# Kernel tuning notes

Hardware: AMD Instinct MI355X
Metric: run time of the kernel (lower is better)

Reference implementation:

```python
import jax, jax.numpy as jnp
import numpy as np
import math

B, H, W, D = 4, 64, 64, 256
N, K, V = 8, 32, 32


def setup_inputs() -> dict:
    key = jax.random.key(0)
    ks = jax.random.split(key, 7)
    blob = jax.random.normal(ks[0], (B, H, W, D), dtype=jnp.float32)
    # 1x1 conv kernels == dense [D, out] matrices; glorot-ish scale
    s = 1.0 / math.sqrt(D)
    wq = jax.random.normal(ks[1], (D, N * K), dtype=jnp.float32) * s
    wk = jax.random.normal(ks[2], (D, N * K), dtype=jnp.float32) * s
    wv = jax.random.normal(ks[3], (D, N * V), dtype=jnp.float32) * s
    bq = jnp.zeros((N * K,), jnp.float32)
    bk = jnp.zeros((N * K,), jnp.float32)
    bv = jnp.zeros((N * V,), jnp.float32)
    return {"blob": blob, "wq": wq, "bq": bq, "wk": wk, "bk": bk, "wv": wv, "bv": bv}


def _maxpool2x2(x):
    # MaxPool2D with pool_size=strides=(2,2), VALID padding, NHWC
    return jax.lax.reduce_window(
        x, -jnp.inf, jax.lax.max,
        window_dimensions=(1, 2, 2, 1), window_strides=(1, 2, 2, 1), padding="VALID")


def reference(blob, wq, bq, wk, bk, wv, bv):
    H2, W2 = H // 2, W // 2
    # pooled query path
    q = _maxpool2x2(blob)                                   # [B,H2,W2,D]
    q = (q @ wq + bq).reshape(B, H2, W2, N, K)              # [B,H2,W2,N,K]
    q = q * (1.0 / math.sqrt(float(K)))
    # key/value paths (1x1 conv == per-pixel matmul); swish on value
    k = (blob @ wk + bk).reshape(B, H * W, N, K)            # [B,HW,N,K]
    v = jax.nn.swish(blob @ wv + bv).reshape(B, H * W, N, V)  # [B,HW,N,V]
    # cross-attention: contract K, outer product of pooled grid with full grid
    scores = jnp.einsum("bhwnk,bink->bhwin", q, k)          # [B,H2,W2,HW,N]
    attn = jax.nn.softmax(scores, axis=3)                   # softmax over HW
    out = jnp.einsum("bhwin,binv->bhwnv", attn, v)          # [B,H2,W2,N,V]
    return out.reshape(B, H2, W2, N * V)
```

## Files before the change

### kernel.cpp

```cpp
#include <hip/hip_runtime.h>


typedef _Float16 f16x8 __attribute__((ext_vector_type(8)));
typedef _Float16 f16x4 __attribute__((ext_vector_type(4)));
typedef float    f32x4 __attribute__((ext_vector_type(4)));

#define F16(x) static_cast<_Float16>(x)

#if __has_builtin(__builtin_amdgcn_exp2f)
#define EXP2(x) __builtin_amdgcn_exp2f(x)
#else
#define EXP2(x) exp2f(x)
#endif

__device__ __forceinline__ void gl_lds16(const void* g, void* l) {
    __builtin_amdgcn_global_load_lds(
        (const __attribute__((address_space(1))) unsigned int*)g,
        (__attribute__((address_space(3))) unsigned int*)l, 16, 0, 0);
}

__global__ __launch_bounds__(256) void prep_kernel(
    const float* __restrict__ wq, const float* __restrict__ wk,
    const float* __restrict__ wv, _Float16* __restrict__ wt) {
    __shared__ float t[32][33];
    const int blk = blockIdx.x;
    const int mat = blk >> 6;
    const int tile = blk & 63;
    const int d0 = (tile >> 3) * 32, o0 = (tile & 7) * 32;
    const float* w = (mat == 0) ? wq : (mat == 1 ? wk : wv);
    const int tx = threadIdx.x & 31, ty = threadIdx.x >> 5;
#pragma unroll
    for (int i = 0; i < 4; ++i)
        t[ty + i * 8][tx] = w[(d0 + ty + i * 8) * 256 + o0 + tx];
    __syncthreads();
#pragma unroll
    for (int i = 0; i < 4; ++i)
        wt[(mat << 16) + (o0 + ty + i * 8) * 256 + d0 + tx] = (_Float16)t[tx][ty + i * 8];
}

__global__ __launch_bounds__(256) void proj_kernel(
    const float* __restrict__ blob, const _Float16* __restrict__ wt,
    const float* __restrict__ bq, const float* __restrict__ bk, const float* __restrict__ bv,
    _Float16* __restrict__ qo, _Float16* __restrict__ ko, _Float16* __restrict__ vo) {
    __shared__ __align__(16) char atile[2][4096];

    const int tid = threadIdx.x;
    const int lane = tid & 63, wid = tid >> 6;
    const int quad = lane >> 4, l16 = lane & 15;
    int jb = blockIdx.x;
    int job, rowblk;
    if (jb < 64)       { job = 0; rowblk = jb; }
    else if (jb < 320) { job = 1; rowblk = jb - 64; }
    else               { job = 2; rowblk = jb - 320; }
    const int rowbase = rowblk * 64;
    const int colbase = wid * 64;
    const _Float16* wmat = wt + ((size_t)job << 16);
    const float* bias = (job == 0) ? bq : (job == 1 ? bk : bv);

    const int srow = tid >> 2, sc8 = tid & 3;
    const int sslot = srow * 4 + ((sc8 + (srow >> 2)) & 3);
    const float* aptr;
    if (job == 0) {
        const int grow = rowbase + srow;
        const int bb = grow >> 10, y = (grow >> 5) & 31, x = grow & 31;
        aptr = blob + (((bb * 64 + 2 * y) * 64) + 2 * x) * 256 + sc8 * 8;
    } else {
        aptr = blob + (size_t)(rowbase + srow) * 256 + sc8 * 8;
    }

    const _Float16* wptr[4];
#pragma unroll
    for (int nt = 0; nt < 4; ++nt)
        wptr[nt] = wmat + (size_t)(colbase + nt * 16 + l16) * 256 + quad * 8;

    const int aread = l16 * 64 + ((quad + (l16 >> 2)) & 3) * 16;

    f32x4 acc[4][4];
#pragma unroll
    for (int mc = 0; mc < 4; ++mc)
#pragma unroll
        for (int nt = 0; nt < 4; ++nt) acc[mc][nt] = (f32x4){0.f, 0.f, 0.f, 0.f};

    f16x8 wf[2][4];
    float4 ar[2][2];

    auto A_LOAD = [&](int t, float4* dst) {
        const float* p = aptr + t * 32;
        if (job == 0) {
            float4 a0 = *(const float4*)(p);
            float4 a1 = *(const float4*)(p + 4);
            float4 b0 = *(const float4*)(p + 256);
            float4 b1 = *(const float4*)(p + 260);
            float4 c0 = *(const float4*)(p + 16384);
            float4 c1 = *(const float4*)(p + 16388);
            float4 d0 = *(const float4*)(p + 16640);
            float4 d1 = *(const float4*)(p + 16644);
            dst[0].x = fmaxf(fmaxf(a0.x, b0.x), fmaxf(c0.x, d0.x));
            dst[0].y = fmaxf(fmaxf(a0.y, b0.y), fmaxf(c0.y, d0.y));
            dst[0].z = fmaxf(fmaxf(a0.z, b0.z), fmaxf(c0.z, d0.z));
            dst[0].w = fmaxf(fmaxf(a0.w, b0.w), fmaxf(c0.w, d0.w));
            dst[1].x = fmaxf(fmaxf(a1.x, b1.x), fmaxf(c1.x, d1.x));
            dst[1].y = fmaxf(fmaxf(a1.y, b1.y), fmaxf(c1.y, d1.y));
            dst[1].z = fmaxf(fmaxf(a1.z, b1.z), fmaxf(c1.z, d1.z));
            dst[1].w = fmaxf(fmaxf(a1.w, b1.w), fmaxf(c1.w, d1.w));
        } else {
            dst[0] = *(const float4*)(p);
            dst[1] = *(const float4*)(p + 4);
        }
    };
    auto A_WRITE = [&](int buf, const float4* src) {
        auto c0 = __builtin_amdgcn_cvt_pkrtz(src[0].x, src[0].y);
        auto c1 = __builtin_amdgcn_cvt_pkrtz(src[0].z, src[0].w);
        auto c2 = __builtin_amdgcn_cvt_pkrtz(src[1].x, src[1].y);
        auto c3 = __builtin_amdgcn_cvt_pkrtz(src[1].z, src[1].w);
        f16x8 v = {F16(c0[0]), F16(c0[1]), F16(c1[0]), F16(c1[1]),
                   F16(c2[0]), F16(c2[1]), F16(c3[0]), F16(c3[1])};
        *(f16x8*)(atile[buf] + sslot * 16) = v;
    };
    auto W_LOAD = [&](int t, f16x8* dst) {
#pragma unroll
        for (int nt = 0; nt < 4; ++nt) dst[nt] = *(const f16x8*)(wptr[nt] + t * 32);
    };

    W_LOAD(0, wf[0]);
    A_LOAD(0, ar[0]);
    A_WRITE(0, ar[0]);
    A_LOAD(1, ar[1]);
    asm volatile("s_waitcnt lgkmcnt(0)\n\ts_barrier" ::: "memory");

#pragma unroll
    for (int s = 0; s < 8; ++s) {
        if (s < 7) W_LOAD(s + 1, wf[(s + 1) & 1]);
        f16x8 af[4];
#pragma unroll
        for (int mc = 0; mc < 4; ++mc)
            af[mc] = *(const f16x8*)(atile[s & 1] + mc * 1024 + aread);
#pragma unroll
        for (int mc = 0; mc < 4; ++mc)
#pragma unroll
            for (int nt = 0; nt < 4; ++nt)
                acc[mc][nt] = __builtin_amdgcn_mfma_f32_16x16x32_f16(
                    af[mc], wf[s & 1][nt], acc[mc][nt], 0, 0, 0);
        if (s < 7) A_WRITE((s + 1) & 1, ar[(s + 1) & 1]);
        if (s < 6) A_LOAD(s + 2, ar[s & 1]);
        if (s < 7) asm volatile("s_waitcnt lgkmcnt(0)\n\ts_barrier" ::: "memory");
    }

#pragma unroll
    for (int nt = 0; nt < 4; ++nt) {
        const int o = colbase + nt * 16 + l16;
        const float bs = bias[o];
        const int nh = o >> 5, kk = o & 31;
#pragma unroll
        for (int mc = 0; mc < 4; ++mc) {
            if (job == 0) {
#pragma unroll
                for (int r = 0; r < 4; ++r) {
                    const int grow = rowbase + mc * 16 + quad * 4 + r;
                    const float x = (acc[mc][nt][r] + bs) * 0.25503508f;
                    const int bb = grow >> 10, mm = grow & 1023;
                    qo[(((bb * 8 + nh) * 1024 + mm) << 5) + kk] = (_Float16)x;
                }
            } else if (job == 1) {
#pragma unroll
                for (int r = 0; r < 4; ++r) {
                    const int grow = rowbase + mc * 16 + quad * 4 + r;
                    const float x = acc[mc][nt][r] + bs;
                    const int bb = grow >> 12, ii = grow & 4095;
                    ko[(((bb * 8 + nh) * 4096 + ii) << 5) + kk] = (_Float16)x;
                }
            } else {
                const int grow0 = rowbase + mc * 16 + quad * 4;
                const int bb = grow0 >> 12, i0 = grow0 & 4095;
                f16x4 pv;
#pragma unroll
                for (int r = 0; r < 4; ++r) {
                    float x = acc[mc][nt][r] + bs;
                    const float sg = 1.0f / (1.0f + __expf(-x));
                    pv[r] = (_Float16)(x * sg);
                }
                *(f16x4*)(vo + (((size_t)(bb * 8 + nh) * 32 + kk) << 12) + i0) = pv;
            }
        }
    }
}

__global__ __launch_bounds__(512, 4) void attn_kernel(
    const _Float16* __restrict__ qb,
    const _Float16* __restrict__ kb,
    const _Float16* __restrict__ vt,
    float* __restrict__ out) {
    __shared__ __align__(16) char pool[49152];

    const int tid = threadIdx.x;
    const int lane = tid & 63, wid = tid >> 6;
    const int quad = lane >> 4, l16 = lane & 15;
    const int bn = blockIdx.x & 31, mt = blockIdx.x >> 5;
    const int b = bn >> 3, n = bn & 7;
    const int m0 = mt * 64;
    const int rg = wid & 3, kc = wid >> 2;

    const _Float16* gsrc[2];
    int ldsoff[2], adv[2];
#pragma unroll
    for (int jj = 0; jj < 2; ++jj) {
        const int j = wid + jj * 8;
        const int kcj = j >> 3, sub = j & 7;
        const int gl = (sub & 3) * 64 + lane;
        if (sub < 4) {
            const int k = gl >> 2, c = ((gl & 3) - (k >> 2)) & 3;
            gsrc[jj]   = kb + ((size_t)bn << 17) + (size_t)(kcj * 2048 + k) * 32 + c * 8;
            ldsoff[jj] = kcj * 24576 + gl * 16;
            adv[jj] = 2048;
        } else {
            const int v = gl >> 3, c = ((gl & 7) - v) & 7;
            gsrc[jj]   = vt + ((size_t)bn << 17) + (size_t)v * 4096 + kcj * 2048 + c * 8;
            ldsoff[jj] = kcj * 24576 + 4096 + gl * 16;
            adv[jj] = 64;
        }
    }

    const f16x8 qf = *(const f16x8*)(qb + (((size_t)(bn << 10) + m0 + rg * 16 + l16) << 5) + quad * 8);

    const int kread = kc * 24576 + l16 * 64 + ((quad + (l16 >> 2)) & 3) * 16;
    const int vread = kc * 24576 + 4096 + l16 * 128 + (quad & 1) * 8;
    const int r0 = (quad >> 1) + l16;

#pragma unroll
    for (int p = 0; p < 2; ++p)
#pragma unroll
        for (int jj = 0; jj < 2; ++jj) {
            gl_lds16(gsrc[jj], pool + ldsoff[jj] + p * 8192);
            gsrc[jj] += adv[jj];
        }
    asm volatile("s_waitcnt vmcnt(2)\n\ts_barrier" ::: "memory");

    f32x4 acc0 = (f32x4){0.f, 0.f, 0.f, 0.f};
    f32x4 acc1 = acc0;
    float ps0 = 0.f;

    for (int s = 0; s < 32; ++s) {
        if (s < 30) {
            const int nb = ((s + 2) % 3) * 8192;
#pragma unroll
            for (int jj = 0; jj < 2; ++jj) {
                gl_lds16(gsrc[jj], pool + ldsoff[jj] + nb);
                gsrc[jj] += adv[jj];
            }
        }
        const char* kbase = pool + kread + (s % 3) * 8192;
        const char* vbase = pool + vread + (s % 3) * 8192;
#pragma unroll
        for (int tloc = 0; tloc < 4; ++tloc) {
            const f16x8 kf = *(const f16x8*)(kbase + tloc * 1024);
            const int rot = ((2 * tloc + r0) & 7) * 16;
            const f16x4 va0 = *(const f16x4*)(vbase + rot);
            const f16x4 va1 = *(const f16x4*)(vbase + rot + 2048);

            f32x4 s0 = __builtin_amdgcn_mfma_f32_16x16x32_f16(kf, qf, (f32x4){0.f,0.f,0.f,0.f}, 0, 0, 0);
            const float p0 = EXP2(s0[0]), p1 = EXP2(s0[1]), p2 = EXP2(s0[2]), p3 = EXP2(s0[3]);
            ps0 += (p0 + p1) + (p2 + p3);
            auto e0 = __builtin_amdgcn_cvt_pkrtz(p0, p1);
            auto e1 = __builtin_amdgcn_cvt_pkrtz(p2, p3);
            const f16x4 pb = {F16(e0[0]), F16(e0[1]), F16(e1[0]), F16(e1[1])};
            acc0 = __builtin_amdgcn_mfma_f32_16x16x16f16(va0, pb, acc0, 0, 0, 0);
            acc1 = __builtin_amdgcn_mfma_f32_16x16x16f16(va1, pb, acc1, 0, 0, 0);
        }
        if (s < 30)       asm volatile("s_waitcnt vmcnt(2)\n\ts_barrier" ::: "memory");
        else if (s == 30) asm volatile("s_waitcnt vmcnt(0)\n\ts_barrier" ::: "memory");
        else              asm volatile("s_barrier" ::: "memory");
    }

    float* num = (float*)pool;
    float* den = (float*)(pool + 64 * 33 * 4);
    for (int i = tid; i < 64 * 33 + 64; i += 512) ((float*)pool)[i] = 0.f;
    __syncthreads();

    ps0 += __shfl_xor(ps0, 16); ps0 += __shfl_xor(ps0, 32);

    const int m = rg * 16 + l16;
#pragma unroll
    for (int r = 0; r < 4; ++r) {
        atomicAdd(&num[m * 33 + quad * 4 + r], acc0[r]);
        atomicAdd(&num[m * 33 + 16 + quad * 4 + r], acc1[r]);
    }
    if (quad == 0) atomicAdd(&den[m], ps0);
    __syncthreads();

    {
        const int mloc = tid >> 3, v4 = (tid & 7) * 4;
        const float inv = 1.0f / den[mloc];
        const float* nr = num + mloc * 33 + v4;
        float4 o = {nr[0] * inv, nr[1] * inv, nr[2] * inv, nr[3] * inv};
        *(float4*)(out + (((size_t)(b << 10) + m0 + mloc) << 8) + n * 32 + v4) = o;
    }
}

extern "C" void kernel_launch(void* const* d_in, const int* in_sizes, int n_in,
                              void* d_out, int out_size, void* d_ws, size_t ws_size,
                              hipStream_t stream) {
    const float* blob = (const float*)d_in[0];
    const float* wq = (const float*)d_in[1];
    const float* bq = (const float*)d_in[2];
    const float* wk = (const float*)d_in[3];
    const float* bk = (const float*)d_in[4];
    const float* wv = (const float*)d_in[5];
    const float* bv = (const float*)d_in[6];
    float* out = (float*)d_out;

    char* ws = (char*)d_ws;
    _Float16* wt = (_Float16*)(ws);
    _Float16* ko = (_Float16*)(ws + 393216);
    _Float16* vo = (_Float16*)(ws + 8781824);
    _Float16* qo = (_Float16*)(ws + 17170432);

    prep_kernel<<<192, 256, 0, stream>>>(wq, wk, wv, wt);
    proj_kernel<<<576, 256, 0, stream>>>(blob, wt, bq, bk, bv, qo, ko, vo);
    attn_kernel<<<512, 512, 0, stream>>>(qo, ko, vo, out);
}
```

Measured before the change: 137.2 us.

## Give each wave a private key slice and pre-swizzle V into fragment layout

The projection kernel now writes V directly in the per-lane MFMA fragment order. Each attention wave then owns a contiguous 512-key slice and streams it through its own 4-stage LDS ring. Each wave processes all four 16-row query groups against its K/V tile, so the per-step block-wide barriers are replaced by per-wave vmcnt waits, and fragments are read with single 16-byte loads. This adds accumulator registers and 64KB of LDS per block, which may lower occupancy.

```diff
diff --git a/kernel.cpp b/kernel.cpp
--- a/kernel.cpp
+++ b/kernel.cpp
@@ -179,7 +179,8 @@
                     const float sg = 1.0f / (1.0f + __expf(-x));
                     pv[r] = (_Float16)(x * sg);
                 }
-                *(f16x4*)(vo + (((size_t)(bb * 8 + nh) * 32 + kk) << 12) + i0) = pv;
+                *(f16x4*)(vo + (size_t)(bb * 8 + nh) * 131072 + (i0 >> 4) * 512
+                             + ((kk & 15) + quad * 16) * 8 + (kk >> 4) * 4) = pv;
             }
         }
     }
@@ -188,9 +189,9 @@
 __global__ __launch_bounds__(512, 4) void attn_kernel(
     const _Float16* __restrict__ qb,
     const _Float16* __restrict__ kb,
-    const _Float16* __restrict__ vt,
+    const _Float16* __restrict__ vf,
     float* __restrict__ out) {
-    __shared__ __align__(16) char pool[49152];
+    __shared__ __align__(16) char pool[65536];
 
     const int tid = threadIdx.x;
     const int lane = tid & 63, wid = tid >> 6;
@@ -198,93 +199,88 @@
     const int bn = blockIdx.x & 31, mt = blockIdx.x >> 5;
     const int b = bn >> 3, n = bn & 7;
     const int m0 = mt * 64;
-    const int rg = wid & 3, kc = wid >> 2;
-
-    const _Float16* gsrc[2];
-    int ldsoff[2], adv[2];
-#pragma unroll
-    for (int jj = 0; jj < 2; ++jj) {
-        const int j = wid + jj * 8;
-        const int kcj = j >> 3, sub = j & 7;
-        const int gl = (sub & 3) * 64 + lane;
-        if (sub < 4) {
-            const int k = gl >> 2, c = ((gl & 3) - (k >> 2)) & 3;
-            gsrc[jj]   = kb + ((size_t)bn << 17) + (size_t)(kcj * 2048 + k) * 32 + c * 8;
-            ldsoff[jj] = kcj * 24576 + gl * 16;
-            adv[jj] = 2048;
+    const int key0 = wid << 9;
+
+    char* const lds0 = pool + wid * 8192;
+
+    const _Float16* kp = kb + ((size_t)bn << 17)
+                            + (size_t)(key0 + (lane & 15)) * 32 + (lane >> 4) * 8;
+    const _Float16* vp = vf + ((size_t)bn << 17) + (size_t)(key0 >> 4) * 512 + lane * 8;
+
+    f16x8 qf[4];
+#pragma unroll
+    for (int rg = 0; rg < 4; ++rg)
+        qf[rg] = *(const f16x8*)(qb + (((size_t)(bn << 10) + m0 + rg * 16 + l16) << 5) + quad * 8);
+
+#pragma unroll
+    for (int p = 0; p < 3; ++p) {
+        gl_lds16(kp, lds0 + p * 2048);        kp += 512;
+        gl_lds16(vp, lds0 + p * 2048 + 1024); vp += 512;
+    }
+
+    f32x4 acc[4][2];
+#pragma unroll
+    for (int rg = 0; rg < 4; ++rg) {
+        acc[rg][0] = (f32x4){0.f, 0.f, 0.f, 0.f};
+        acc[rg][1] = acc[rg][0];
+    }
+    float ps[4] = {0.f, 0.f, 0.f, 0.f};
+
+#pragma unroll 4
+    for (int s = 0; s < 32; ++s) {
+        if (s < 29) {
+            char* nb = lds0 + ((s + 3) & 3) * 2048;
+            gl_lds16(kp, nb);        kp += 512;
+            gl_lds16(vp, nb + 1024); vp += 512;
+            asm volatile("s_waitcnt vmcnt(6)" ::: "memory");
+        } else if (s == 29) {
+            asm volatile("s_waitcnt vmcnt(4)" ::: "memory");
+        } else if (s == 30) {
+            asm volatile("s_waitcnt vmcnt(2)" ::: "memory");
         } else {
-            const int v = gl >> 3, c = ((gl & 7) - v) & 7;
-            gsrc[jj]   = vt + ((size_t)bn << 17) + (size_t)v * 4096 + kcj * 2048 + c * 8;
-            ldsoff[jj] = kcj * 24576 + 4096 + gl * 16;
-            adv[jj] = 64;
-        }
-    }
-
-    const f16x8 qf = *(const f16x8*)(qb + (((size_t)(bn << 10) + m0 + rg * 16 + l16) << 5) + quad * 8);
-
-    const int kread = kc * 24576 + l16 * 64 + ((quad + (l16 >> 2)) & 3) * 16;
-    const int vread = kc * 24576 + 4096 + l16 * 128 + (quad & 1) * 8;
-    const int r0 = (quad >> 1) + l16;
-
-#pragma unroll
-    for (int p = 0; p < 2; ++p)
-#pragma unroll
-        for (int jj = 0; jj < 2; ++jj) {
-            gl_lds16(gsrc[jj], pool + ldsoff[jj] + p * 8192);
-            gsrc[jj] += adv[jj];
-        }
-    asm volatile("s_waitcnt vmcnt(2)\n\ts_barrier" ::: "memory");
-
-    f32x4 acc0 = (f32x4){0.f, 0.f, 0.f, 0.f};
-    f32x4 acc1 = acc0;
-    float ps0 = 0.f;
-
-    for (int s = 0; s < 32; ++s) {
-        if (s < 30) {
-            const int nb = ((s + 2) % 3) * 8192;
-#pragma unroll
-            for (int jj = 0; jj < 2; ++jj) {
-                gl_lds16(gsrc[jj], pool + ldsoff[jj] + nb);
-                gsrc[jj] += adv[jj];
-            }
-        }
-        const char* kbase = pool + kread + (s % 3) * 8192;
-        const char* vbase = pool + vread + (s % 3) * 8192;
-#pragma unroll
-        for (int tloc = 0; tloc < 4; ++tloc) {
-            const f16x8 kf = *(const f16x8*)(kbase + tloc * 1024);
-            const int rot = ((2 * tloc + r0) & 7) * 16;
-            const f16x4 va0 = *(const f16x4*)(vbase + rot);
-            const f16x4 va1 = *(const f16x4*)(vbase + rot + 2048);
-
-            f32x4 s0 = __builtin_amdgcn_mfma_f32_16x16x32_f16(kf, qf, (f32x4){0.f,0.f,0.f,0.f}, 0, 0, 0);
+            asm volatile("s_waitcnt vmcnt(0)" ::: "memory");
+        }
+        const char* base = lds0 + (s & 3) * 2048;
+        const f16x8 kf = *(const f16x8*)(base + lane * 16);
+        const f16x8 vv = *(const f16x8*)(base + 1024 + lane * 16);
+        const f16x4 va0 = {vv[0], vv[1], vv[2], vv[3]};
+        const f16x4 va1 = {vv[4], vv[5], vv[6], vv[7]};
+#pragma unroll
+        for (int rg = 0; rg < 4; ++rg) {
+            f32x4 s0 = __builtin_amdgcn_mfma_f32_16x16x32_f16(kf, qf[rg], (f32x4){0.f,0.f,0.f,0.f}, 0, 0, 0);
             const float p0 = EXP2(s0[0]), p1 = EXP2(s0[1]), p2 = EXP2(s0[2]), p3 = EXP2(s0[3]);
-            ps0 += (p0 + p1) + (p2 + p3);
+            ps[rg] += (p0 + p1) + (p2 + p3);
             auto e0 = __builtin_amdgcn_cvt_pkrtz(p0, p1);
             auto e1 = __builtin_amdgcn_cvt_pkrtz(p2, p3);
             const f16x4 pb = {F16(e0[0]), F16(e0[1]), F16(e1[0]), F16(e1[1])};
-            acc0 = __builtin_amdgcn_mfma_f32_16x16x16f16(va0, pb, acc0, 0, 0, 0);
-            acc1 = __builtin_amdgcn_mfma_f32_16x16x16f16(va1, pb, acc1, 0, 0, 0);
-        }
-        if (s < 30)       asm volatile("s_waitcnt vmcnt(2)\n\ts_barrier" ::: "memory");
-        else if (s == 30) asm volatile("s_waitcnt vmcnt(0)\n\ts_barrier" ::: "memory");
-        else              asm volatile("s_barrier" ::: "memory");
-    }
-
+            acc[rg][0] = __builtin_amdgcn_mfma_f32_16x16x16f16(va0, pb, acc[rg][0], 0, 0, 0);
+            acc[rg][1] = __builtin_amdgcn_mfma_f32_16x16x16f16(va1, pb, acc[rg][1], 0, 0, 0);
+        }
+    }
+
+    asm volatile("s_waitcnt vmcnt(0)" ::: "memory");
+    __syncthreads();
     float* num = (float*)pool;
     float* den = (float*)(pool + 64 * 33 * 4);
     for (int i = tid; i < 64 * 33 + 64; i += 512) ((float*)pool)[i] = 0.f;
     __syncthreads();
 
-    ps0 += __shfl_xor(ps0, 16); ps0 += __shfl_xor(ps0, 32);
-
-    const int m = rg * 16 + l16;
-#pragma unroll
-    for (int r = 0; r < 4; ++r) {
-        atomicAdd(&num[m * 33 + quad * 4 + r], acc0[r]);
-        atomicAdd(&num[m * 33 + 16 + quad * 4 + r], acc1[r]);
-    }
-    if (quad == 0) atomicAdd(&den[m], ps0);
+#pragma unroll
+    for (int rg = 0; rg < 4; ++rg) {
+        ps[rg] += __shfl_xor(ps[rg], 16);
+        ps[rg] += __shfl_xor(ps[rg], 32);
+    }
+
+#pragma unroll
+    for (int rg = 0; rg < 4; ++rg) {
+        const int m = rg * 16 + l16;
+#pragma unroll
+        for (int r = 0; r < 4; ++r) {
+            atomicAdd(&num[m * 33 + quad * 4 + r], acc[rg][0][r]);
+            atomicAdd(&num[m * 33 + 16 + quad * 4 + r], acc[rg][1][r]);
+        }
+        if (quad == 0) atomicAdd(&den[m], ps[rg]);
+    }
     __syncthreads();
 
     {
```

After: 162.3 us. +18.3%, slower.

## Store K and V in MFMA-fragment order so LDS reads are contiguous

Applied to the files above, without the earlier changes.

The projection kernel now writes V in a pre-swizzled fragment layout that matches the per-lane MFMA operand order. The attention kernel's async global-to-LDS copies become plain contiguous 1 KB chunks for K and V with a uniform advance, and each lane reads K and V with one 16-byte LDS load at lane*16 instead of rotated, swizzled addresses and two 8-byte V loads. This cuts address arithmetic and LDS read instructions in the inner loop. The trade-off is that the producer's scattered stores change pattern, and bank-conflict behaviour now depends on the linear lane layout.

```diff
diff --git a/kernel.cpp b/kernel.cpp
--- a/kernel.cpp
+++ b/kernel.cpp
@@ -179,7 +179,8 @@
                     const float sg = 1.0f / (1.0f + __expf(-x));
                     pv[r] = (_Float16)(x * sg);
                 }
-                *(f16x4*)(vo + (((size_t)(bb * 8 + nh) * 32 + kk) << 12) + i0) = pv;
+                *(f16x4*)(vo + (size_t)(bb * 8 + nh) * 131072 + (i0 >> 4) * 512
+                             + ((kk & 15) + quad * 16) * 8 + (kk >> 4) * 4) = pv;
             }
         }
     }
@@ -188,7 +189,7 @@
 __global__ __launch_bounds__(512, 4) void attn_kernel(
     const _Float16* __restrict__ qb,
     const _Float16* __restrict__ kb,
-    const _Float16* __restrict__ vt,
+    const _Float16* __restrict__ vf,
     float* __restrict__ out) {
     __shared__ __align__(16) char pool[49152];
 
@@ -201,37 +202,32 @@
     const int rg = wid & 3, kc = wid >> 2;
 
     const _Float16* gsrc[2];
-    int ldsoff[2], adv[2];
+    int ldsoff[2];
 #pragma unroll
     for (int jj = 0; jj < 2; ++jj) {
         const int j = wid + jj * 8;
         const int kcj = j >> 3, sub = j & 7;
-        const int gl = (sub & 3) * 64 + lane;
         if (sub < 4) {
-            const int k = gl >> 2, c = ((gl & 3) - (k >> 2)) & 3;
-            gsrc[jj]   = kb + ((size_t)bn << 17) + (size_t)(kcj * 2048 + k) * 32 + c * 8;
-            ldsoff[jj] = kcj * 24576 + gl * 16;
-            adv[jj] = 2048;
+            gsrc[jj] = kb + ((size_t)bn << 17)
+                     + (size_t)(kcj * 2048 + sub * 16 + (lane & 15)) * 32 + (lane >> 4) * 8;
+            ldsoff[jj] = kcj * 24576 + sub * 1024;
         } else {
-            const int v = gl >> 3, c = ((gl & 7) - v) & 7;
-            gsrc[jj]   = vt + ((size_t)bn << 17) + (size_t)v * 4096 + kcj * 2048 + c * 8;
-            ldsoff[jj] = kcj * 24576 + 4096 + gl * 16;
-            adv[jj] = 64;
+            gsrc[jj] = vf + ((size_t)bn << 17)
+                     + (size_t)(kcj * 128 + (sub - 4)) * 512 + lane * 8;
+            ldsoff[jj] = kcj * 24576 + 4096 + (sub - 4) * 1024;
         }
     }
 
     const f16x8 qf = *(const f16x8*)(qb + (((size_t)(bn << 10) + m0 + rg * 16 + l16) << 5) + quad * 8);
 
-    const int kread = kc * 24576 + l16 * 64 + ((quad + (l16 >> 2)) & 3) * 16;
-    const int vread = kc * 24576 + 4096 + l16 * 128 + (quad & 1) * 8;
-    const int r0 = (quad >> 1) + l16;
+    const int rbase = kc * 24576 + lane * 16;
 
 #pragma unroll
     for (int p = 0; p < 2; ++p)
 #pragma unroll
         for (int jj = 0; jj < 2; ++jj) {
             gl_lds16(gsrc[jj], pool + ldsoff[jj] + p * 8192);
-            gsrc[jj] += adv[jj];
+            gsrc[jj] += 2048;
         }
     asm volatile("s_waitcnt vmcnt(2)\n\ts_barrier" ::: "memory");
 
@@ -245,17 +241,16 @@
 #pragma unroll
             for (int jj = 0; jj < 2; ++jj) {
                 gl_lds16(gsrc[jj], pool + ldsoff[jj] + nb);
-                gsrc[jj] += adv[jj];
+                gsrc[jj] += 2048;
             }
         }
-        const char* kbase = pool + kread + (s % 3) * 8192;
-        const char* vbase = pool + vread + (s % 3) * 8192;
+        const char* base = pool + rbase + (s % 3) * 8192;
 #pragma unroll
         for (int tloc = 0; tloc < 4; ++tloc) {
-            const f16x8 kf = *(const f16x8*)(kbase + tloc * 1024);
-            const int rot = ((2 * tloc + r0) & 7) * 16;
-            const f16x4 va0 = *(const f16x4*)(vbase + rot);
-            const f16x4 va1 = *(const f16x4*)(vbase + rot + 2048);
+            const f16x8 kf = *(const f16x8*)(base + tloc * 1024);
+            const f16x8 vv = *(const f16x8*)(base + 4096 + tloc * 1024);
+            const f16x4 va0 = {vv[0], vv[1], vv[2], vv[3]};
+            const f16x4 va1 = {vv[4], vv[5], vv[6], vv[7]};
 
             f32x4 s0 = __builtin_amdgcn_mfma_f32_16x16x32_f16(kf, qf, (f32x4){0.f,0.f,0.f,0.f}, 0, 0, 0);
             const float p0 = EXP2(s0[0]), p1 = EXP2(s0[1]), p2 = EXP2(s0[2]), p3 = EXP2(s0[3]);
```

After: 133.8 us. 2.5% less time.
